# Kernel tuning notes

Measured on AMD Instinct MI355X. Metric: run time of the kernel, lower is better.

The kernel has to match this reference:

```python
import jax, jax.numpy as jnp
import numpy as np

B, T, C, H, W = 1, 16, 320, 16, 16
HEADS, DIM_HEAD, NREG = 8, 40, 1
L = T * H * W  # 4096


def setup_inputs() -> dict:
    key = jax.random.key(0)
    ks = jax.random.split(key, 8)
    features = jax.random.normal(ks[0], (B, T, C, H, W), jnp.float32)
    # epipolar geometry mask: True = attend. randint 0/1 per spec.
    attn_mask = jax.random.randint(ks[1], (B, L, L), 0, 2) == 1
    s = 0.02
    Wq = jax.random.normal(ks[2], (C, HEADS * DIM_HEAD), jnp.float32) * s
    Wk = jax.random.normal(ks[3], (C, HEADS * DIM_HEAD), jnp.float32) * s
    Wv = jax.random.normal(ks[4], (C, HEADS * DIM_HEAD), jnp.float32) * s
    reg_tokens = jax.random.normal(ks[5], (1, NREG, C), jnp.float32)
    Wo = jax.random.normal(ks[6], (HEADS * DIM_HEAD, C), jnp.float32) * s
    bo = jnp.zeros((C,), jnp.float32)
    return {"features": features, "attn_mask": attn_mask, "Wq": Wq, "Wk": Wk,
            "Wv": Wv, "reg_tokens": reg_tokens, "Wo": Wo, "bo": bo}


def reference(features, attn_mask, Wq, Wk, Wv, reg_tokens, Wo, bo):
    b, t, c, h, w = features.shape
    # B T C H W -> B (T H W) C
    x = features.transpose(0, 1, 3, 4, 2).reshape(b, t * h * w, c)
    context = jnp.concatenate(
        [jnp.broadcast_to(reg_tokens, (b, NREG, c)), x], axis=1)
    # pad mask: register tokens always visible (True)
    mask = jnp.pad(attn_mask, ((0, 0), (0, 0), (NREG, 0)), constant_values=True)
    # projections, split heads: B L (H D) -> B H L D
    def heads(y):
        return y.reshape(b, y.shape[1], HEADS, DIM_HEAD).transpose(0, 2, 1, 3)
    q = heads(x @ Wq)
    k = heads(context @ Wk)
    v = heads(context @ Wv)
    scale = DIM_HEAD ** -0.5  # SDPA default scale
    scores = jnp.einsum('bhqd,bhkd->bhqk', q, k) * scale
    neg = jnp.finfo(scores.dtype).min
    scores = jnp.where(mask[:, None, :, :], scores, neg)
    attn = jax.nn.softmax(scores, axis=-1)
    out = jnp.einsum('bhqk,bhkd->bhqd', attn, v)
    out = out.transpose(0, 2, 1, 3).reshape(b, t * h * w, HEADS * DIM_HEAD)
    out = out @ Wo + bo
    # B (T H W) C -> (B H W) T C
    out = out.reshape(b, t, h, w, c).transpose(0, 2, 3, 1, 4)
    return out.reshape(b * h * w, t, c)
```

## Files before the change

### kernel.cpp

```cpp
#include <hip/hip_runtime.h>
#include <hip/hip_bf16.h>
#include <math.h>

#define CDIM 320
#define LQ   4096
#define LKTX 4097
#define NH   8
#define DH   40
#define NWORDS 65
#define NSPLIT 4
#define CBROWS 4224

typedef __attribute__((ext_vector_type(8))) short short8;
typedef __attribute__((ext_vector_type(4))) short short4v;
typedef __attribute__((ext_vector_type(4))) float f32x4;

#define MFMA16(a, b, c) __builtin_amdgcn_mfma_f32_16x16x16bf16_1k(a, b, c, 0, 0, 0)
#define MFMA32(a, b, c) __builtin_amdgcn_mfma_f32_16x16x32_bf16(a, b, c, 0, 0, 0)

#define QSCALE ((float)(0.15811388300841897 * 1.4426950408889634))

__global__ __launch_bounds__(256) void prep(
    const float* __restrict__ feat, const float* __restrict__ reg,
    const float* __restrict__ Wq, const float* __restrict__ Wk,
    const float* __restrict__ Wv, const float* __restrict__ Wo,
    const int* __restrict__ mask, unsigned long long* __restrict__ packed,
    __hip_bfloat16* __restrict__ ctxb, __hip_bfloat16* __restrict__ Wt,
    __hip_bfloat16* __restrict__ Wot) {
    __shared__ float xs[64 * 65];
    int b = blockIdx.x, t = threadIdx.x;
    if (b < 16384) {
        int wid = b * 4 + (t >> 6);
        int j = t & 63;
        int q = wid >> 4, g = wid & 15;
        const uint4* m4 = (const uint4*)(mask + (size_t)q * 4096 + g * 256);
        uint4 mv = m4[j];
        unsigned long long b0 = __ballot(mv.x != 0);
        unsigned long long b1 = __ballot(mv.y != 0);
        unsigned long long b2 = __ballot(mv.z != 0);
        unsigned long long b3 = __ballot(mv.w != 0);
        unsigned long long carry =
            (g == 0) ? 1ull
                     : (unsigned long long)(mask[(size_t)q * 4096 + g * 256 - 1] != 0);
        unsigned long long b3s = (b3 << 1) | carry;
        if (j < 4) {
            int sh = j * 16;
            unsigned long long w = ((b3s >> sh) & 0xFFFFull) |
                                   (((b0 >> sh) & 0xFFFFull) << 16) |
                                   (((b1 >> sh) & 0xFFFFull) << 32) |
                                   (((b2 >> sh) & 0xFFFFull) << 48);
            packed[(size_t)q * NWORDS + g * 4 + j] = w;
        }
        if (j == 4 && g == 15) packed[(size_t)q * NWORDS + 64] = b3 >> 63;
    } else if (b < 16704) {
        int bb = b - 16384;
        int tt = bb & 15, cg = (bb >> 4) % 5, hg = (bb >> 4) / 5;
        int c0 = cg * 64, hw0 = hg * 64;
        int cl = t >> 6, hwl = t & 63;
#pragma unroll
        for (int i = 0; i < 16; i++) {
            int c = cl * 16 + i;
            xs[c * 65 + hwl] = feat[(size_t)(tt * CDIM + c0 + c) * 256 + hw0 + hwl];
        }
        __syncthreads();
        int cq = t >> 6;
        int row = tt * 256 + hw0 + hwl;
        short8 v0, v1;
#pragma unroll
        for (int j = 0; j < 8; j++) {
            __hip_bfloat16 b0 = __float2bfloat16(xs[(cq * 16 + j) * 65 + hwl]);
            __hip_bfloat16 b1 = __float2bfloat16(xs[(cq * 16 + 8 + j) * 65 + hwl]);
            v0[j] = *(short*)&b0;
            v1[j] = *(short*)&b1;
        }
        short* dst = (short*)ctxb + (size_t)(1 + row) * CDIM + c0 + cq * 16;
        *(short8*)dst = v0;
        *(short8*)(dst + 8) = v1;
    } else {
        int idx = (b - 16704) * 256 + t;
        if (idx < 960 * 320) {
            int n = idx / 320, k = idx % 320;
            float v;
            if (n < 320)      v = Wq[k * 320 + n] * QSCALE;
            else if (n < 640) v = Wk[k * 320 + (n - 320)];
            else              v = Wv[k * 320 + (n - 640)];
            Wt[n * 320 + k] = __float2bfloat16(v);
        }
        if (idx < 320 * 320) {
            int n = idx / 320, k = idx % 320;
            Wot[n * 320 + k] = __float2bfloat16(Wo[k * 320 + n]);
        }
        if (idx < 320) ctxb[idx] = __float2bfloat16(reg[idx]);
    }
}

__global__ __launch_bounds__(256) void qkv_gemm(
    const __hip_bfloat16* __restrict__ Ab, const __hip_bfloat16* __restrict__ Btb,
    __hip_bfloat16* __restrict__ Cbo) {
    __shared__ short As[64 * 72];
    __shared__ short Bs[128 * 72];
    const short* A  = (const short*)Ab;
    const short* Bt = (const short*)Btb;
    int t = threadIdx.x;
    int wv = t >> 6, lane = t & 63, quad = lane >> 4, l16 = lane & 15;
    int m0 = blockIdx.y * 64, n0 = blockIdx.x * 128;

    f32x4 acc[8];
#pragma unroll
    for (int ct = 0; ct < 8; ct++)
#pragma unroll
        for (int r = 0; r < 4; r++) acc[ct][r] = 0.f;

    for (int k0 = 0; k0 < 320; k0 += 64) {
        uint4 av[2], bv[4];
#pragma unroll
        for (int i = 0; i < 2; i++) {
            int c = t + i * 256;
            int row = c >> 3, kc = (c & 7) * 8;
            av[i] = make_uint4(0, 0, 0, 0);
            if (m0 + row < LKTX)
                av[i] = *(const uint4*)(A + (size_t)(m0 + row) * 320 + k0 + kc);
        }
#pragma unroll
        for (int i = 0; i < 4; i++) {
            int c = t + i * 256;
            int row = c >> 3, kc = (c & 7) * 8;
            bv[i] = make_uint4(0, 0, 0, 0);
            if (n0 + row < 960)
                bv[i] = *(const uint4*)(Bt + (size_t)(n0 + row) * 320 + k0 + kc);
        }
        __syncthreads();
#pragma unroll
        for (int i = 0; i < 2; i++) {
            int c = t + i * 256;
            *(uint4*)&As[(c >> 3) * 72 + (c & 7) * 8] = av[i];
        }
#pragma unroll
        for (int i = 0; i < 4; i++) {
            int c = t + i * 256;
            *(uint4*)&Bs[(c >> 3) * 72 + (c & 7) * 8] = bv[i];
        }
        __syncthreads();
        short8 a0 = *(const short8*)&As[(wv * 16 + l16) * 72 + quad * 8];
        short8 a1 = *(const short8*)&As[(wv * 16 + l16) * 72 + 32 + quad * 8];
#pragma unroll
        for (int ct = 0; ct < 8; ct++) {
            short8 b0 = *(const short8*)&Bs[(ct * 16 + l16) * 72 + quad * 8];
            short8 b1 = *(const short8*)&Bs[(ct * 16 + l16) * 72 + 32 + quad * 8];
            acc[ct] = MFMA32(a0, b0, acc[ct]);
            acc[ct] = MFMA32(a1, b1, acc[ct]);
        }
        __syncthreads();
    }
#pragma unroll
    for (int ct = 0; ct < 8; ct++)
#pragma unroll
        for (int r = 0; r < 4; r++) {
            int m = m0 + wv * 16 + quad * 4 + r;
            int n = n0 + ct * 16 + l16;
            if (n < 960)
                Cbo[(size_t)m * 960 + n] = __float2bfloat16(acc[ct][r]);
        }
}

__global__ __launch_bounds__(256, 4) void flash_attn(
    const __hip_bfloat16* __restrict__ Cbh,
    const unsigned long long* __restrict__ packed,
    float* __restrict__ Opart, float* __restrict__ l_arr) {
    __shared__ short Ks[2 * 64 * 72];
    __shared__ short Vs[2 * 48 * 72];

    int t = threadIdx.x;
    int wv = t >> 6, lane = t & 63;
    int quad = lane >> 4, l16 = lane & 15;
    int h = blockIdx.y, s = blockIdx.z;
    int q0 = blockIdx.x * 128 + wv * 32;
    int kt0 = (s == 0) ? 0 : 16 * s + 1;
    int nkt = s ? 16 : 17;
    const short* Cb = (const short*)Cbh;

    for (int i = t; i < 64 * 24; i += 256) {
        int rr = i / 24, c = 40 + i % 24;
        Ks[rr * 72 + c] = 0;
        Ks[4608 + rr * 72 + c] = 0;
    }
    for (int i = t; i < 8 * 72; i += 256) {
        int rr = i / 72, c = i % 72;
        short v = (rr == 0 && c < 64) ? (short)0x3F80 : (short)0;
        Vs[(40 + rr) * 72 + c] = v;
        Vs[3456 + (40 + rr) * 72 + c] = v;
    }

    short8 qa[2][2];
#pragma unroll
    for (int qs = 0; qs < 2; qs++) {
        const short* qp = Cb + (size_t)(q0 + qs * 16 + l16 + 1) * 960 + h * DH;
        qa[qs][0] = *(const short8*)(qp + quad * 8);
        short8 z = {0, 0, 0, 0, 0, 0, 0, 0};
        qa[qs][1] = (quad == 0) ? *(const short8*)(qp + 32) : z;
    }

    int key0 = t / 5, cc0 = t - 5 * key0;
    int t2 = t + 256;
    int key1 = t2 / 5, cc1 = t2 - 5 * key1;
    bool has2 = (t < 64);
    const short* pK0 = Cb + (size_t)(kt0 * 64 + key0) * 960 + 320 + h * DH + cc0 * 8;
    const short* pV0 = Cb + (size_t)(kt0 * 64 + key0) * 960 + 640 + h * DH + cc0 * 8;
    const short* pK1 = Cb + (size_t)(kt0 * 64 + key1) * 960 + 320 + h * DH + cc1 * 8;
    const short* pV1 = Cb + (size_t)(kt0 * 64 + key1) * 960 + 640 + h * DH + cc1 * 8;
    const unsigned long long* pM0 = packed + (size_t)(q0 + l16) * NWORDS + kt0;
    const unsigned long long* pM1 = packed + (size_t)(q0 + 16 + l16) * NWORDS + kt0;

    uint4 rk0 = *(const uint4*)pK0;  pK0 += 61440;
    uint4 rv0 = *(const uint4*)pV0;  pV0 += 61440;
    uint4 rk1 = make_uint4(0, 0, 0, 0), rv1 = make_uint4(0, 0, 0, 0);
    if (has2) { rk1 = *(const uint4*)pK1; rv1 = *(const uint4*)pV1; }
    pK1 += 61440; pV1 += 61440;
    unsigned long long wq0 = *pM0++;
    unsigned long long wq1 = *pM1++;

    f32x4 accO[2][3];
#pragma unroll
    for (int qs = 0; qs < 2; qs++)
#pragma unroll
        for (int dt = 0; dt < 3; dt++)
#pragma unroll
            for (int r = 0; r < 4; r++) accO[qs][dt][r] = 0.f;

    for (int it = 0; it < nkt; it++) {
        int ko = (it & 1) * 4608, vo = (it & 1) * 3456;
        *(uint4*)&Ks[ko + key0 * 72 + cc0 * 8] = rk0;
        {
            const short* ds = (const short*)&rv0;
#pragma unroll
            for (int u = 0; u < 8; u++) Vs[vo + (cc0 * 8 + u) * 72 + key0] = ds[u];
        }
        if (has2) {
            *(uint4*)&Ks[ko + key1 * 72 + cc1 * 8] = rk1;
            const short* ds = (const short*)&rv1;
#pragma unroll
            for (int u = 0; u < 8; u++) Vs[vo + (cc1 * 8 + u) * 72 + key1] = ds[u];
        }
        unsigned long long mw0 = wq0, mw1 = wq1;
        rk0 = *(const uint4*)pK0;  pK0 += 61440;
        rv0 = *(const uint4*)pV0;  pV0 += 61440;
        if (has2) { rk1 = *(const uint4*)pK1; rv1 = *(const uint4*)pV1; }
        pK1 += 61440; pV1 += 61440;
        wq0 = *pM0++;
        wq1 = *pM1++;
        __syncthreads();

        const short* KB = &Ks[ko];
        const short* VB = &Vs[vo];
        unsigned lo[2], hi[2];
        lo[0] = (unsigned)(mw0 >> quad);
        hi[0] = (unsigned)(mw0 >> (quad + 32));
        lo[1] = (unsigned)(mw1 >> quad);
        hi[1] = (unsigned)(mw1 >> (quad + 32));

        short4v pf[2][4];
#pragma unroll
        for (int ct = 0; ct < 4; ct++) {
            short8 kb0 = *(const short8*)&KB[(ct * 16 + l16) * 72 + quad * 8];
            short8 kb1 = *(const short8*)&KB[(ct * 16 + l16) * 72 + 32 + quad * 8];
#pragma unroll
            for (int qs = 0; qs < 2; qs++) {
                f32x4 S = {0.f, 0.f, 0.f, 0.f};
                S = MFMA32(kb0, qa[qs][0], S);
                S = MFMA32(kb1, qa[qs][1], S);
                float p0 = __builtin_amdgcn_exp2f(S[0]);
                float p1 = __builtin_amdgcn_exp2f(S[1]);
                float p2 = __builtin_amdgcn_exp2f(S[2]);
                float p3 = __builtin_amdgcn_exp2f(S[3]);
                p0 = ((lo[qs] >> (4 * ct)) & 1u) ? p0 : 0.f;
                p1 = ((lo[qs] >> (4 * ct + 16)) & 1u) ? p1 : 0.f;
                p2 = ((hi[qs] >> (4 * ct)) & 1u) ? p2 : 0.f;
                p3 = ((hi[qs] >> (4 * ct + 16)) & 1u) ? p3 : 0.f;
                unsigned u0 = __float_as_uint(p0) + 0x8000u;
                unsigned u1 = __float_as_uint(p1) + 0x8000u;
                unsigned u2 = __float_as_uint(p2) + 0x8000u;
                unsigned u3 = __float_as_uint(p3) + 0x8000u;
                uint2 pk = make_uint2((u0 >> 16) | (u1 & 0xFFFF0000u),
                                      (u2 >> 16) | (u3 & 0xFFFF0000u));
                pf[qs][ct] = *(short4v*)&pk;
            }
        }

#pragma unroll
        for (int dt = 0; dt < 3; dt++) {
#pragma unroll
            for (int ct = 0; ct < 4; ct++) {
                short4v vf = *(const short4v*)&VB[(dt * 16 + l16) * 72 + ct * 16 + quad * 4];
                accO[0][dt] = MFMA16(vf, pf[0][ct], accO[0][dt]);
                accO[1][dt] = MFMA16(vf, pf[1][ct], accO[1][dt]);
            }
        }
    }

#pragma unroll
    for (int qs = 0; qs < 2; qs++) {
        int q = q0 + qs * 16 + l16;
        size_t base = ((size_t)(s * NH + h) * LQ + q) * DH;
        float4 f0 = make_float4(accO[qs][0][0], accO[qs][0][1], accO[qs][0][2], accO[qs][0][3]);
        float4 f1 = make_float4(accO[qs][1][0], accO[qs][1][1], accO[qs][1][2], accO[qs][1][3]);
        *(float4*)&Opart[base + quad * 4] = f0;
        *(float4*)&Opart[base + 16 + quad * 4] = f1;
        if (quad < 2) {
            float4 f2 = make_float4(accO[qs][2][0], accO[qs][2][1], accO[qs][2][2], accO[qs][2][3]);
            *(float4*)&Opart[base + 32 + quad * 4] = f2;
        }
        if (quad == 2) l_arr[(size_t)(s * NH + h) * LQ + q] = accO[qs][2][0];
    }
}

__global__ __launch_bounds__(256) void out_gemm(
    const float* __restrict__ Opart, const float* __restrict__ l_arr,
    const __hip_bfloat16* __restrict__ Wotb, float* __restrict__ C,
    const float* __restrict__ bias) {
    __shared__ short As[64 * 72];
    __shared__ short Bs[64 * 72];
    const short* Bt = (const short*)Wotb;
    int t = threadIdx.x;
    int wv = t >> 6, lane = t & 63, quad = lane >> 4, l16 = lane & 15;
    int m0 = blockIdx.y * 64, n0 = blockIdx.x * 64;

    f32x4 acc[4];
#pragma unroll
    for (int ct = 0; ct < 4; ct++)
#pragma unroll
        for (int r = 0; r < 4; r++) acc[ct][r] = 0.f;

    for (int k0 = 0; k0 < 5; k0++) {
        uint4 av[2], bv[2];
#pragma unroll
        for (int i = 0; i < 2; i++) {
            int cidx = t + i * 256;
            int row = cidx >> 3, cl = (cidx & 7) * 8;
            int c = k0 * 64 + cl;
            int hh = c / 40, d = c % 40;
            int q = m0 + row;
            float ls = 0.f;
            float vals[8] = {0, 0, 0, 0, 0, 0, 0, 0};
#pragma unroll
            for (int sp = 0; sp < NSPLIT; sp++) {
                size_t rbase = ((size_t)(sp * NH + hh) * LQ + q) * DH + d;
                float4 a = *(const float4*)&Opart[rbase];
                float4 b = *(const float4*)&Opart[rbase + 4];
                vals[0] += a.x; vals[1] += a.y; vals[2] += a.z; vals[3] += a.w;
                vals[4] += b.x; vals[5] += b.y; vals[6] += b.z; vals[7] += b.w;
                ls += l_arr[(size_t)(sp * NH + hh) * LQ + q];
            }
            float inv = 1.f / ls;
            unsigned pk[4];
#pragma unroll
            for (int u = 0; u < 4; u++) {
                unsigned e0 = __float_as_uint(vals[2 * u] * inv) + 0x8000u;
                unsigned e1 = __float_as_uint(vals[2 * u + 1] * inv) + 0x8000u;
                pk[u] = (e0 >> 16) | (e1 & 0xFFFF0000u);
            }
            av[i] = make_uint4(pk[0], pk[1], pk[2], pk[3]);
            bv[i] = *(const uint4*)(Bt + (size_t)(n0 + row) * 320 + k0 * 64 + cl);
        }
        __syncthreads();
#pragma unroll
        for (int i = 0; i < 2; i++) {
            int cidx = t + i * 256;
            *(uint4*)&As[(cidx >> 3) * 72 + (cidx & 7) * 8] = av[i];
            *(uint4*)&Bs[(cidx >> 3) * 72 + (cidx & 7) * 8] = bv[i];
        }
        __syncthreads();
        short8 a0 = *(const short8*)&As[(wv * 16 + l16) * 72 + quad * 8];
        short8 a1 = *(const short8*)&As[(wv * 16 + l16) * 72 + 32 + quad * 8];
#pragma unroll
        for (int ct = 0; ct < 4; ct++) {
            short8 b0 = *(const short8*)&Bs[(ct * 16 + l16) * 72 + quad * 8];
            short8 b1 = *(const short8*)&Bs[(ct * 16 + l16) * 72 + 32 + quad * 8];
            acc[ct] = MFMA32(a0, b0, acc[ct]);
            acc[ct] = MFMA32(a1, b1, acc[ct]);
        }
        __syncthreads();
    }
#pragma unroll
    for (int ct = 0; ct < 4; ct++)
#pragma unroll
        for (int r = 0; r < 4; r++) {
            int m = m0 + wv * 16 + quad * 4 + r;
            int n = n0 + ct * 16 + l16;
            int rp = (m & 255) * 16 + (m >> 8);
            C[(size_t)rp * CDIM + n] = acc[ct][r] + bias[n];
        }
}

extern "C" void kernel_launch(void* const* d_in, const int* in_sizes, int n_in,
                              void* d_out, int out_size, void* d_ws, size_t ws_size,
                              hipStream_t stream) {
    const float* feat = (const float*)d_in[0];
    const int*   mask = (const int*)d_in[1];
    const float* Wq   = (const float*)d_in[2];
    const float* Wk   = (const float*)d_in[3];
    const float* Wv   = (const float*)d_in[4];
    const float* reg  = (const float*)d_in[5];
    const float* Wo   = (const float*)d_in[6];
    const float* bo   = (const float*)d_in[7];
    float* out = (float*)d_out;

    char* p = (char*)d_ws;
    auto alloc = [&](size_t bytes) {
        char* r = p;
        p += (bytes + 255) & ~(size_t)255;
        return r;
    };
    __hip_bfloat16* ctxb = (__hip_bfloat16*)alloc((size_t)LKTX * CDIM * 2);
    __hip_bfloat16* Cb   = (__hip_bfloat16*)alloc((size_t)CBROWS * 960 * 2);
    __hip_bfloat16* Wt   = (__hip_bfloat16*)alloc((size_t)960 * 320 * 2);
    __hip_bfloat16* Wot  = (__hip_bfloat16*)alloc((size_t)320 * 320 * 2);
    unsigned long long* packed =
        (unsigned long long*)alloc(((size_t)LQ * NWORDS + 64) * 8);
    float* Opart = (float*)alloc((size_t)NSPLIT * NH * LQ * DH * 4);
    float* l_arr = (float*)alloc((size_t)NSPLIT * NH * LQ * 4);

    prep<<<17904, 256, 0, stream>>>(feat, reg, Wq, Wk, Wv, Wo, mask, packed,
                                    ctxb, Wt, Wot);
    qkv_gemm<<<dim3(8, 65), 256, 0, stream>>>(ctxb, Wt, Cb);
    flash_attn<<<dim3(32, NH, NSPLIT), 256, 0, stream>>>(Cb, packed, Opart, l_arr);
    out_gemm<<<dim3(5, 64), 256, 0, stream>>>(Opart, l_arr, Wot, out, bo);
}
```

Before: 221.3 us.

## Widen flash-attn query tile to 64 per wave, split keys 8-way, add combine kernel

Each wave in the attention kernel now handles 64 queries instead of 32, so every K/V tile loaded into shared memory is reused across four query subtiles. The QK product switches to 16x16x16 MFMA with K-dim padding shrunk from 64 to 48, and the V LDS stride changes to 68. The key range is split 8 ways instead of 4, which keeps the grid size up. The split-K reduction moves out of the output GEMM into a separate combine kernel that writes bf16 activations. The trade-off is higher register pressure (occupancy hint drops to 3), twice the partial-output traffic, and one extra kernel launch.

```diff
diff --git a/kernel.cpp b/kernel.cpp
--- a/kernel.cpp
+++ b/kernel.cpp
@@ -8,7 +8,7 @@
 #define NH   8
 #define DH   40
 #define NWORDS 65
-#define NSPLIT 4
+#define NSPLIT 8
 #define CBROWS 4224
 
 typedef __attribute__((ext_vector_type(8))) short short8;
@@ -163,41 +163,42 @@
         }
 }
 
-__global__ __launch_bounds__(256, 4) void flash_attn(
+__global__ __launch_bounds__(256, 3) void flash_attn(
     const __hip_bfloat16* __restrict__ Cbh,
     const unsigned long long* __restrict__ packed,
     float* __restrict__ Opart, float* __restrict__ l_arr) {
     __shared__ short Ks[2 * 64 * 72];
-    __shared__ short Vs[2 * 48 * 72];
+    __shared__ short Vs[2 * 48 * 68];
 
     int t = threadIdx.x;
     int wv = t >> 6, lane = t & 63;
     int quad = lane >> 4, l16 = lane & 15;
     int h = blockIdx.y, s = blockIdx.z;
-    int q0 = blockIdx.x * 128 + wv * 32;
-    int kt0 = (s == 0) ? 0 : 16 * s + 1;
-    int nkt = s ? 16 : 17;
+    int q0 = blockIdx.x * 256 + wv * 64;
+    int kt0 = s ? 8 * s + 1 : 0;
+    int nkt = s ? 8 : 9;
     const short* Cb = (const short*)Cbh;
 
-    for (int i = t; i < 64 * 24; i += 256) {
-        int rr = i / 24, c = 40 + i % 24;
+    for (int i = t; i < 64 * 8; i += 256) {
+        int rr = i >> 3, c = 40 + (i & 7);
         Ks[rr * 72 + c] = 0;
-        Ks[4608 + rr * 72 + c] = 0;
-    }
-    for (int i = t; i < 8 * 72; i += 256) {
-        int rr = i / 72, c = i % 72;
+        Ks[64 * 72 + rr * 72 + c] = 0;
+    }
+    for (int i = t; i < 8 * 68; i += 256) {
+        int rr = i / 68, c = i % 68;
         short v = (rr == 0 && c < 64) ? (short)0x3F80 : (short)0;
-        Vs[(40 + rr) * 72 + c] = v;
-        Vs[3456 + (40 + rr) * 72 + c] = v;
-    }
-
-    short8 qa[2][2];
-#pragma unroll
-    for (int qs = 0; qs < 2; qs++) {
+        Vs[(40 + rr) * 68 + c] = v;
+        Vs[48 * 68 + (40 + rr) * 68 + c] = v;
+    }
+
+    short4v qb[4][3];
+#pragma unroll
+    for (int qs = 0; qs < 4; qs++) {
         const short* qp = Cb + (size_t)(q0 + qs * 16 + l16 + 1) * 960 + h * DH;
-        qa[qs][0] = *(const short8*)(qp + quad * 8);
-        short8 z = {0, 0, 0, 0, 0, 0, 0, 0};
-        qa[qs][1] = (quad == 0) ? *(const short8*)(qp + 32) : z;
+        qb[qs][0] = *(const short4v*)(qp + quad * 4);
+        qb[qs][1] = *(const short4v*)(qp + 16 + quad * 4);
+        short4v z = {0, 0, 0, 0};
+        qb[qs][2] = (quad < 2) ? *(const short4v*)(qp + 32 + quad * 4) : z;
     }
 
     int key0 = t / 5, cc0 = t - 5 * key0;
@@ -208,70 +209,81 @@
     const short* pV0 = Cb + (size_t)(kt0 * 64 + key0) * 960 + 640 + h * DH + cc0 * 8;
     const short* pK1 = Cb + (size_t)(kt0 * 64 + key1) * 960 + 320 + h * DH + cc1 * 8;
     const short* pV1 = Cb + (size_t)(kt0 * 64 + key1) * 960 + 640 + h * DH + cc1 * 8;
-    const unsigned long long* pM0 = packed + (size_t)(q0 + l16) * NWORDS + kt0;
-    const unsigned long long* pM1 = packed + (size_t)(q0 + 16 + l16) * NWORDS + kt0;
+    const unsigned long long* pM[4];
+#pragma unroll
+    for (int qs = 0; qs < 4; qs++)
+        pM[qs] = packed + (size_t)(q0 + qs * 16 + l16) * NWORDS + kt0;
 
     uint4 rk0 = *(const uint4*)pK0;  pK0 += 61440;
     uint4 rv0 = *(const uint4*)pV0;  pV0 += 61440;
     uint4 rk1 = make_uint4(0, 0, 0, 0), rv1 = make_uint4(0, 0, 0, 0);
     if (has2) { rk1 = *(const uint4*)pK1; rv1 = *(const uint4*)pV1; }
     pK1 += 61440; pV1 += 61440;
-    unsigned long long wq0 = *pM0++;
-    unsigned long long wq1 = *pM1++;
-
-    f32x4 accO[2][3];
-#pragma unroll
-    for (int qs = 0; qs < 2; qs++)
+    unsigned long long wq[4];
+#pragma unroll
+    for (int qs = 0; qs < 4; qs++) wq[qs] = *pM[qs]++;
+
+    f32x4 accO[4][3];
+#pragma unroll
+    for (int qs = 0; qs < 4; qs++)
 #pragma unroll
         for (int dt = 0; dt < 3; dt++)
 #pragma unroll
             for (int r = 0; r < 4; r++) accO[qs][dt][r] = 0.f;
 
     for (int it = 0; it < nkt; it++) {
-        int ko = (it & 1) * 4608, vo = (it & 1) * 3456;
+        int ko = (it & 1) * (64 * 72), vo = (it & 1) * (48 * 68);
         *(uint4*)&Ks[ko + key0 * 72 + cc0 * 8] = rk0;
         {
             const short* ds = (const short*)&rv0;
 #pragma unroll
-            for (int u = 0; u < 8; u++) Vs[vo + (cc0 * 8 + u) * 72 + key0] = ds[u];
+            for (int u = 0; u < 8; u++) Vs[vo + (cc0 * 8 + u) * 68 + key0] = ds[u];
         }
         if (has2) {
             *(uint4*)&Ks[ko + key1 * 72 + cc1 * 8] = rk1;
             const short* ds = (const short*)&rv1;
 #pragma unroll
-            for (int u = 0; u < 8; u++) Vs[vo + (cc1 * 8 + u) * 72 + key1] = ds[u];
-        }
-        unsigned long long mw0 = wq0, mw1 = wq1;
+            for (int u = 0; u < 8; u++) Vs[vo + (cc1 * 8 + u) * 68 + key1] = ds[u];
+        }
+        unsigned long long mw[4];
+#pragma unroll
+        for (int qs = 0; qs < 4; qs++) mw[qs] = wq[qs];
         rk0 = *(const uint4*)pK0;  pK0 += 61440;
         rv0 = *(const uint4*)pV0;  pV0 += 61440;
         if (has2) { rk1 = *(const uint4*)pK1; rv1 = *(const uint4*)pV1; }
         pK1 += 61440; pV1 += 61440;
-        wq0 = *pM0++;
-        wq1 = *pM1++;
+#pragma unroll
+        for (int qs = 0; qs < 4; qs++) wq[qs] = *pM[qs]++;
         __syncthreads();
 
         const short* KB = &Ks[ko];
         const short* VB = &Vs[vo];
-        unsigned lo[2], hi[2];
-        lo[0] = (unsigned)(mw0 >> quad);
-        hi[0] = (unsigned)(mw0 >> (quad + 32));
-        lo[1] = (unsigned)(mw1 >> quad);
-        hi[1] = (unsigned)(mw1 >> (quad + 32));
-
-        short4v pf[2][4];
+        unsigned lo[4], hi[4];
+#pragma unroll
+        for (int qs = 0; qs < 4; qs++) {
+            lo[qs] = (unsigned)(mw[qs] >> quad);
+            hi[qs] = (unsigned)(mw[qs] >> (quad + 32));
+        }
+
 #pragma unroll
         for (int ct = 0; ct < 4; ct++) {
-            short8 kb0 = *(const short8*)&KB[(ct * 16 + l16) * 72 + quad * 8];
-            short8 kb1 = *(const short8*)&KB[(ct * 16 + l16) * 72 + 32 + quad * 8];
-#pragma unroll
-            for (int qs = 0; qs < 2; qs++) {
-                f32x4 S = {0.f, 0.f, 0.f, 0.f};
-                S = MFMA32(kb0, qa[qs][0], S);
-                S = MFMA32(kb1, qa[qs][1], S);
-                float p0 = __builtin_amdgcn_exp2f(S[0]);
-                float p1 = __builtin_amdgcn_exp2f(S[1]);
-                float p2 = __builtin_amdgcn_exp2f(S[2]);
-                float p3 = __builtin_amdgcn_exp2f(S[3]);
+            f32x4 S[4];
+#pragma unroll
+            for (int qs = 0; qs < 4; qs++) S[qs] = f32x4{0.f, 0.f, 0.f, 0.f};
+#pragma unroll
+            for (int kc = 0; kc < 3; kc++) {
+                short4v kf = *(const short4v*)&KB[(ct * 16 + l16) * 72 + kc * 16 + quad * 4];
+#pragma unroll
+                for (int qs = 0; qs < 4; qs++)
+                    S[qs] = MFMA16(kf, qb[qs][kc], S[qs]);
+            }
+            short4v pf[4];
+#pragma unroll
+            for (int qs = 0; qs < 4; qs++) {
+                float p0 = __builtin_amdgcn_exp2f(S[qs][0]);
+                float p1 = __builtin_amdgcn_exp2f(S[qs][1]);
+                float p2 = __builtin_amdgcn_exp2f(S[qs][2]);
+                float p3 = __builtin_amdgcn_exp2f(S[qs][3]);
                 p0 = ((lo[qs] >> (4 * ct)) & 1u) ? p0 : 0.f;
                 p1 = ((lo[qs] >> (4 * ct + 16)) & 1u) ? p1 : 0.f;
                 p2 = ((hi[qs] >> (4 * ct)) & 1u) ? p2 : 0.f;
@@ -282,23 +294,20 @@
                 unsigned u3 = __float_as_uint(p3) + 0x8000u;
                 uint2 pk = make_uint2((u0 >> 16) | (u1 & 0xFFFF0000u),
                                       (u2 >> 16) | (u3 & 0xFFFF0000u));
-                pf[qs][ct] = *(short4v*)&pk;
+                pf[qs] = *(short4v*)&pk;
             }
-        }
-
-#pragma unroll
-        for (int dt = 0; dt < 3; dt++) {
-#pragma unroll
-            for (int ct = 0; ct < 4; ct++) {
-                short4v vf = *(const short4v*)&VB[(dt * 16 + l16) * 72 + ct * 16 + quad * 4];
-                accO[0][dt] = MFMA16(vf, pf[0][ct], accO[0][dt]);
-                accO[1][dt] = MFMA16(vf, pf[1][ct], accO[1][dt]);
+#pragma unroll
+            for (int dt = 0; dt < 3; dt++) {
+                short4v vf = *(const short4v*)&VB[(dt * 16 + l16) * 68 + ct * 16 + quad * 4];
+#pragma unroll
+                for (int qs = 0; qs < 4; qs++)
+                    accO[qs][dt] = MFMA16(vf, pf[qs], accO[qs][dt]);
             }
         }
     }
 
 #pragma unroll
-    for (int qs = 0; qs < 2; qs++) {
+    for (int qs = 0; qs < 4; qs++) {
         int q = q0 + qs * 16 + l16;
         size_t base = ((size_t)(s * NH + h) * LQ + q) * DH;
         float4 f0 = make_float4(accO[qs][0][0], accO[qs][0][1], accO[qs][0][2], accO[qs][0][3]);
@@ -313,13 +322,42 @@
     }
 }
 
+__global__ __launch_bounds__(256) void combine(
+    const float* __restrict__ Opart, const float* __restrict__ l_arr,
+    __hip_bfloat16* __restrict__ aob) {
+    int idx = blockIdx.x * 256 + threadIdx.x;
+    if (idx >= NH * LQ * 5) return;
+    int dg = idx % 5;
+    int hq = idx / 5;
+    int q = hq & (LQ - 1), h = hq >> 12;
+    float ls = 0.f;
+    float vals[8] = {0, 0, 0, 0, 0, 0, 0, 0};
+#pragma unroll
+    for (int sp = 0; sp < NSPLIT; sp++) {
+        size_t rbase = ((size_t)(sp * NH + h) * LQ + q) * DH + dg * 8;
+        float4 a = *(const float4*)&Opart[rbase];
+        float4 b = *(const float4*)&Opart[rbase + 4];
+        vals[0] += a.x; vals[1] += a.y; vals[2] += a.z; vals[3] += a.w;
+        vals[4] += b.x; vals[5] += b.y; vals[6] += b.z; vals[7] += b.w;
+        ls += l_arr[(size_t)(sp * NH + h) * LQ + q];
+    }
+    float inv = 1.f / ls;
+    short8 o;
+#pragma unroll
+    for (int j = 0; j < 8; j++) {
+        unsigned u = __float_as_uint(vals[j] * inv) + 0x8000u;
+        o[j] = (short)(u >> 16);
+    }
+    *(short8*)((short*)aob + (size_t)q * CDIM + h * DH + dg * 8) = o;
+}
+
 __global__ __launch_bounds__(256) void out_gemm(
-    const float* __restrict__ Opart, const float* __restrict__ l_arr,
-    const __hip_bfloat16* __restrict__ Wotb, float* __restrict__ C,
-    const float* __restrict__ bias) {
+    const __hip_bfloat16* __restrict__ Ab, const __hip_bfloat16* __restrict__ Btb,
+    float* __restrict__ C, const float* __restrict__ bias) {
     __shared__ short As[64 * 72];
     __shared__ short Bs[64 * 72];
-    const short* Bt = (const short*)Wotb;
+    const short* A  = (const short*)Ab;
+    const short* Bt = (const short*)Btb;
     int t = threadIdx.x;
     int wv = t >> 6, lane = t & 63, quad = lane >> 4, l16 = lane & 15;
     int m0 = blockIdx.y * 64, n0 = blockIdx.x * 64;
@@ -330,43 +368,21 @@
 #pragma unroll
         for (int r = 0; r < 4; r++) acc[ct][r] = 0.f;
 
-    for (int k0 = 0; k0 < 5; k0++) {
+    for (int k0 = 0; k0 < 320; k0 += 64) {
         uint4 av[2], bv[2];
 #pragma unroll
         for (int i = 0; i < 2; i++) {
-            int cidx = t + i * 256;
-            int row = cidx >> 3, cl = (cidx & 7) * 8;
-            int c = k0 * 64 + cl;
-            int hh = c / 40, d = c % 40;
-            int q = m0 + row;
-            float ls = 0.f;
-            float vals[8] = {0, 0, 0, 0, 0, 0, 0, 0};
-#pragma unroll
-            for (int sp = 0; sp < NSPLIT; sp++) {
-                size_t rbase = ((size_t)(sp * NH + hh) * LQ + q) * DH + d;
-                float4 a = *(const float4*)&Opart[rbase];
-                float4 b = *(const float4*)&Opart[rbase + 4];
-                vals[0] += a.x; vals[1] += a.y; vals[2] += a.z; vals[3] += a.w;
-                vals[4] += b.x; vals[5] += b.y; vals[6] += b.z; vals[7] += b.w;
-                ls += l_arr[(size_t)(sp * NH + hh) * LQ + q];
-            }
-            float inv = 1.f / ls;
-            unsigned pk[4];
-#pragma unroll
-            for (int u = 0; u < 4; u++) {
-                unsigned e0 = __float_as_uint(vals[2 * u] * inv) + 0x8000u;
-                unsigned e1 = __float_as_uint(vals[2 * u + 1] * inv) + 0x8000u;
-                pk[u] = (e0 >> 16) | (e1 & 0xFFFF0000u);
-            }
-            av[i] = make_uint4(pk[0], pk[1], pk[2], pk[3]);
-            bv[i] = *(const uint4*)(Bt + (size_t)(n0 + row) * 320 + k0 * 64 + cl);
+            int c = t + i * 256;
+            int row = c >> 3, kc = (c & 7) * 8;
+            av[i] = *(const uint4*)(A + (size_t)(m0 + row) * 320 + k0 + kc);
+            bv[i] = *(const uint4*)(Bt + (size_t)(n0 + row) * 320 + k0 + kc);
         }
         __syncthreads();
 #pragma unroll
         for (int i = 0; i < 2; i++) {
-            int cidx = t + i * 256;
-            *(uint4*)&As[(cidx >> 3) * 72 + (cidx & 7) * 8] = av[i];
-            *(uint4*)&Bs[(cidx >> 3) * 72 + (cidx & 7) * 8] = bv[i];
+            int c = t + i * 256;
+            *(uint4*)&As[(c >> 3) * 72 + (c & 7) * 8] = av[i];
+            *(uint4*)&Bs[(c >> 3) * 72 + (c & 7) * 8] = bv[i];
         }
         __syncthreads();
         short8 a0 = *(const short8*)&As[(wv * 16 + l16) * 72 + quad * 8];
@@ -418,10 +434,12 @@
         (unsigned long long*)alloc(((size_t)LQ * NWORDS + 64) * 8);
     float* Opart = (float*)alloc((size_t)NSPLIT * NH * LQ * DH * 4);
     float* l_arr = (float*)alloc((size_t)NSPLIT * NH * LQ * 4);
+    __hip_bfloat16* aob  = (__hip_bfloat16*)alloc((size_t)LQ * CDIM * 2);
 
     prep<<<17904, 256, 0, stream>>>(feat, reg, Wq, Wk, Wv, Wo, mask, packed,
                                     ctxb, Wt, Wot);
     qkv_gemm<<<dim3(8, 65), 256, 0, stream>>>(ctxb, Wt, Cb);
-    flash_attn<<<dim3(32, NH, NSPLIT), 256, 0, stream>>>(Cb, packed, Opart, l_arr);
-    out_gemm<<<dim3(5, 64), 256, 0, stream>>>(Opart, l_arr, Wot, out, bo);
-}
+    flash_attn<<<dim3(16, NH, NSPLIT), 256, 0, stream>>>(Cb, packed, Opart, l_arr);
+    combine<<<(NH * LQ * 5 + 255) / 256, 256, 0, stream>>>(Opart, l_arr, aob);
+    out_gemm<<<dim3(5, 64), 256, 0, stream>>>(aob, Wot, out, bo);
+}
```

New measurement: 319.1 us. 44.2% more time.
